# Kernel optimization log

Measured on AMD Instinct MI355X. Metric: run time of the kernel, lower is better.

The kernel has to match this reference:

```python
import jax, jax.numpy as jnp
import numpy as np

NUM_HEADS = 16


def setup_inputs() -> dict:
    key = jax.random.key(0)
    ks = jax.random.split(key, 6)
    B, T, C = 2, 1024, 2048
    H, D = NUM_HEADS, C // NUM_HEADS
    Tc = 1024  # cached tokens
    return {
        "x": jax.random.normal(ks[0], (B, T, C), dtype=jnp.float32),
        "cache_k": jax.random.normal(ks[1], (B, H, Tc, D), dtype=jnp.float32),
        "cache_v": jax.random.normal(ks[2], (B, H, Tc, D), dtype=jnp.float32),
        "W_qkv": jax.random.normal(ks[3], (C, 3 * C), dtype=jnp.float32) * (C ** -0.5),
        "W_proj": jax.random.normal(ks[4], (C, C), dtype=jnp.float32) * (C ** -0.5),
        "b_proj": jnp.zeros((C,), dtype=jnp.float32),
        "seq_start": Tc,
    }


def reference(x, cache_k, cache_v, W_qkv, W_proj, b_proj, seq_start):
    B, T, C = x.shape
    H = NUM_HEADS
    D = C // H
    scale = D ** -0.5

    qkv = (x @ W_qkv).reshape(B, T, 3, H, D)
    # (B, H, T, D)
    q = jnp.transpose(qkv[:, :, 0], (0, 2, 1, 3))
    k = jnp.transpose(qkv[:, :, 1], (0, 2, 1, 3))
    v = jnp.transpose(qkv[:, :, 2], (0, 2, 1, 3))

    # append to KV cache along time axis
    k = jnp.concatenate([cache_k, k], axis=2)
    v = jnp.concatenate([cache_v, v], axis=2)
    k_len = k.shape[2]

    # causal mask on absolute positions: query_pos >= key_pos
    query_pos = seq_start + jnp.arange(T)
    key_pos = jnp.arange(k_len)
    causal = query_pos[:, None] >= key_pos[None, :]  # (T, k_len)

    attn = jnp.einsum("bhqd,bhkd->bhqk", q * scale, k)
    attn = jnp.where(causal[None, None], attn, -jnp.inf)
    attn = jax.nn.softmax(attn, axis=-1)

    out = jnp.einsum("bhqk,bhkd->bhqd", attn, v)
    out = jnp.transpose(out, (0, 2, 1, 3)).reshape(B, T, C)
    out = out @ W_proj + b_proj
    return out, k, v
```

## Files before the change

### kernel.cpp

```cpp
#include <hip/hip_runtime.h>
#include <hip/hip_bf16.h>

typedef __attribute__((ext_vector_type(8))) short bf16x8;
typedef __attribute__((ext_vector_type(4))) float f32x4;
typedef __attribute__((ext_vector_type(16))) float f32x16;

#define DI __device__ __forceinline__

static constexpr int Bb  = 2;
static constexpr int Tt  = 1024;
static constexpr int Cc  = 2048;
static constexpr int Hh  = 16;
static constexpr int Dd  = 128;
static constexpr int TC  = 1024;
static constexpr int CTX = 2048;
static constexpr int LDP = 2112;
static constexpr int VS  = 2080;
static constexpr float QSCALE = 0.08838834764831845f;

DI unsigned short f2bf(float f){
  unsigned u = __builtin_bit_cast(unsigned, f);
  u += 0x7FFFu + ((u >> 16) & 1u);
  return (unsigned short)(u >> 16);
}
DI float bf2f(unsigned short s){
  return __builtin_bit_cast(float, (unsigned)s << 16);
}
DI unsigned pk2(float a, float b){
  return (unsigned)f2bf(a) | ((unsigned)f2bf(b) << 16);
}
DI bf16x8 mk4(unsigned a, unsigned b, unsigned c, unsigned d){
  union{ unsigned u[4]; bf16x8 v; } x;
  x.u[0]=a; x.u[1]=b; x.u[2]=c; x.u[3]=d; return x.v;
}
DI f32x16 mfma32(bf16x8 a, bf16x8 b, f32x16 c){
  return __builtin_amdgcn_mfma_f32_32x32x16_bf16(a, b, c, 0, 0, 0);
}
#define MFMA16(a,b,c) __builtin_amdgcn_mfma_f32_16x16x32_bf16(a,b,c,0,0,0)
DI void gld16(const void* g, void* l){
  __builtin_amdgcn_global_load_lds(
      (const __attribute__((address_space(1))) unsigned int*)g,
      (__attribute__((address_space(3))) unsigned int*)l, 16, 0, 0);
}
DI unsigned ldsoff(const void* p){
  return (unsigned)(size_t)(const __attribute__((address_space(3))) void*)p;
}
template<int OFF>
DI bf16x8 dsr(unsigned addr){
  bf16x8 v;
  if constexpr (OFF == 0)
    asm volatile("ds_read_b128 %0, %1" : "=v"(v) : "v"(addr));
  else
    asm volatile("ds_read_b128 %0, %1 offset:%2" : "=v"(v) : "v"(addr), "i"(OFF));
  return v;
}
#define BARNC   asm volatile("s_barrier")
#define LGKM0   asm volatile("s_waitcnt lgkmcnt(0)")
#define VMCNT4  asm volatile("s_waitcnt vmcnt(4)")
#define VMCNT0  asm volatile("s_waitcnt vmcnt(0)")
#define SBAR    __builtin_amdgcn_sched_barrier(0)

DI void transpose_body(const float* in, unsigned short* out,
                       int R, int C, int ostride, int r0, int c0, int mode,
                       unsigned short (*tile)[33]){
  int tx = threadIdx.x & 31, ty = threadIdx.x >> 5;
#pragma unroll
  for(int i=0;i<4;i++){
    int r = r0 + ty + i*8;
    tile[ty + i*8][tx] = f2bf(in[(size_t)r * C + c0 + tx]);
  }
  __syncthreads();
#pragma unroll
  for(int i=0;i<4;i++){
    int c = c0 + ty + i*8;
    int k = r0 + tx;
    int kp;
    if(mode == 0)
      kp = (k & ~24) | ((((k>>3)&3) ^ ((c>>1)&3)) << 3);
    else
      kp = (k & ~56) | ((((k>>3)&7) ^ (c&7)) << 3);
    out[(size_t)c * ostride + kp] = tile[tx][ty + i*8];
  }
}

__global__ __launch_bounds__(256) void fused_pre_k(
    const float* __restrict__ W_qkv, unsigned short* __restrict__ WqkvT,
    const float4* __restrict__ x4, unsigned short* __restrict__ xbf,
    const float4* __restrict__ ck, const float4* __restrict__ cv,
    float4* __restrict__ ok, float4* __restrict__ ov,
    unsigned short* __restrict__ Kws){
  __shared__ unsigned short tile[32][33];
  int bid = blockIdx.x;
  if(bid < 12288){
    int bx = bid % 192, by = bid / 192;
    transpose_body(W_qkv, WqkvT, 2048, 6144, LDP, by*32, bx*32, 0, tile);
  } else if(bid < 16384){
    int idx = (bid - 12288) * 256 + threadIdx.x;
    int m = idx >> 9;
    int c4 = (idx & 511) * 4;
    float4 v = x4[idx];
    int cp = (c4 & ~24) | ((((c4>>3)&3) ^ ((m>>1)&3)) << 3);
    uint2 p; p.x = pk2(v.x, v.y); p.y = pk2(v.z, v.w);
    *(uint2*)(xbf + (size_t)m * LDP + cp) = p;
  } else {
    int idx = (bid - 16384) * 256 + threadIdx.x;
    const int per = TC * Dd / 4;
    int bh = idx / per, r = idx - bh * per;
    int dst = bh * (CTX * Dd / 4) + r;
    float4 kv = ck[idx];
    ok[dst] = kv;
    ov[dst] = cv[idx];
    int key = r >> 5, dq = (r & 31) * 4;
    int dp = (((dq>>3) ^ (key&7)) << 3) | (dq & 7);
    uint2 p; p.x = pk2(kv.x, kv.y); p.y = pk2(kv.z, kv.w);
    *(uint2*)(Kws + ((size_t)bh * CTX + key) * Dd + dp) = p;
  }
}

__global__ __launch_bounds__(256) void fused_mid_k(
    const float* __restrict__ out_v, unsigned short* __restrict__ Vt_ws,
    const float* __restrict__ W_proj, unsigned short* __restrict__ WprojT){
  __shared__ unsigned short tile[32][33];
  int bid = blockIdx.x;
  if(bid < 8192){
    int z = bid >> 8, rem = bid & 255;
    int bx = rem & 3, by = rem >> 2;
    transpose_body(out_v + (size_t)z*2048*128, Vt_ws + (size_t)z*128*VS,
                   2048, 128, VS, by*32, bx*32, 1, tile);
  } else {
    int b2 = bid - 8192;
    int bx = b2 & 63, by = b2 >> 6;
    transpose_body(W_proj, WprojT, 2048, 2048, LDP, by*32, bx*32, 0, tile);
  }
}

template<int EPI, int NT>
__global__ __launch_bounds__(256, 4) void gemm_t(
    const unsigned short* __restrict__ A, const unsigned short* __restrict__ BT,
    unsigned short* __restrict__ q_ws, float* __restrict__ out_k,
    float* __restrict__ out_v, unsigned short* __restrict__ Kws,
    const float* __restrict__ bias, float* __restrict__ outp){
  constexpr int K = 2048;
  __shared__ unsigned short Al[2][128*32];
  __shared__ unsigned short Bl[2][128*32];
  int tid = threadIdx.x, lane = tid & 63, w = tid >> 6;
  int lr = lane & 15, lg = lane >> 4;
  constexpr int NWG = 16 * NT;
  int bid = blockIdx.x;
  int swz = (bid & 7) * (NWG/8) + (bid >> 3);
  int m0 = (swz & 15) * 128;
  int n0 = (swz >> 4) * 128;
  int wr = (w >> 1) * 64, wc = (w & 1) * 64;
  int fsw = (lg ^ ((lr >> 1) & 3)) << 3;

  unsigned baseAb = ldsoff(Al) + (unsigned)(((wr + lr)*32 + fsw)*2);
  unsigned baseBb = ldsoff(Bl) + (unsigned)(((wc + lr)*32 + fsw)*2);

  f32x4 acc[4][4];
#pragma unroll
  for(int i=0;i<4;i++)
#pragma unroll
    for(int j=0;j<4;j++) acc[i][j] = (f32x4){0.f,0.f,0.f,0.f};

  auto stage = [&](int buf, int k0){
#pragma unroll
    for(int li=0; li<2; li++){
      int rb = w*32 + li*16;
      gld16(A  + (size_t)(m0 + rb + (lane>>2))*LDP + k0 + (lane&3)*8, &Al[buf][rb*32]);
      gld16(BT + (size_t)(n0 + rb + (lane>>2))*LDP + k0 + (lane&3)*8, &Bl[buf][rb*32]);
    }
  };
  stage(0, 0);
  int buf = 0;
#pragma unroll 1
  for(int k0 = 0; k0 < K; k0 += 32){
    SBAR;
    if(k0 + 32 < K){
      stage(buf^1, k0 + 32);
      SBAR;
      VMCNT4;
    } else {
      SBAR;
      VMCNT0;
    }
    BARNC;
    unsigned aA = baseAb + (unsigned)buf*8192u;
    unsigned aB = baseBb + (unsigned)buf*8192u;
    bf16x8 af[4], bfr[4];
    af[0]  = dsr<0>(aA);    af[1]  = dsr<1024>(aA);
    af[2]  = dsr<2048>(aA); af[3]  = dsr<3072>(aA);
    bfr[0] = dsr<0>(aB);    bfr[1] = dsr<1024>(aB);
    bfr[2] = dsr<2048>(aB); bfr[3] = dsr<3072>(aB);
    LGKM0;
    SBAR;
    __builtin_amdgcn_s_setprio(1);
#pragma unroll
    for(int mi=0;mi<4;mi++)
#pragma unroll
      for(int ni=0;ni<4;ni++)
        acc[mi][ni] = MFMA16(af[mi], bfr[ni], acc[mi][ni]);
    __builtin_amdgcn_s_setprio(0);
    SBAR;
    BARNC;
    buf ^= 1;
  }

#pragma unroll
  for(int mi=0;mi<4;mi++){
#pragma unroll
    for(int ni=0;ni<4;ni++){
      int n = n0 + wc + ni*16 + lr;
#pragma unroll
      for(int r=0;r<4;r++){
        int mrow = m0 + wr + mi*16 + lg*4 + r;
        float v = acc[mi][ni][r];
        if constexpr (EPI == 0){
          int seg = n >> 11;
          int h = (n >> 7) & 15, d = n & 127;
          int b = mrow >> 10, t = mrow & 1023;
          if(seg == 0){
            q_ws[((size_t)(b*Hh + h)*Tt + t)*Dd + d] = f2bf(v * QSCALE);
          } else if(seg == 1){
            int key = TC + t;
            size_t base = (size_t)(b*Hh + h)*CTX + key;
            out_k[base*Dd + d] = v;
            int dp = (((d>>3) ^ (key&7)) << 3) | (d & 7);
            Kws[base*Dd + dp] = f2bf(v);
          } else {
            out_v[((size_t)(b*Hh + h)*CTX + TC + t)*Dd + d] = v;
          }
        } else {
          outp[(size_t)mrow * Cc + n] = v + bias[n];
        }
      }
    }
  }
}

__global__ __launch_bounds__(256, 2) void attn_k(
    const unsigned short* __restrict__ q_ws,
    const unsigned short* __restrict__ Kws,
    const unsigned short* __restrict__ Vt,
    float* __restrict__ O0, unsigned short* __restrict__ O1b,
    float* __restrict__ ml){
  __shared__ unsigned short Kl[2][64*128];
  __shared__ unsigned short Vl[2][128*64];
  int tid = threadIdx.x, lane = tid & 63, w = tid >> 6;
  int l31 = lane & 31, hi = lane >> 5, r7 = l31 & 7;
  int qt = blockIdx.x, split = blockIdx.y, bh = blockIdx.z;
  int q0b = qt * 128, qw0 = q0b + w * 32;
  const unsigned short* Kb = Kws + (size_t)bh * CTX * Dd;
  const unsigned short* Vb = Vt  + (size_t)bh * Dd * VS;

  const unsigned short* qp = q_ws + ((size_t)bh * Tt + qw0 + l31) * Dd + hi * 8;
  bf16x8 qf[8];
#pragma unroll
  for(int ks=0;ks<8;ks++) qf[ks] = *(const bf16x8*)(qp + ks*16);

  f32x16 o[4];
#pragma unroll
  for(int dt=0;dt<4;dt++)
#pragma unroll
    for(int r=0;r<16;r++) o[dt][r] = 0.f;
  float m = -3e38f, l = 0.f;

  int nts = ((TC + q0b + 128) >> 6) >> 1;

  auto stageK = [&](int buf, int j0){
#pragma unroll
    for(int li=0; li<4; li++){
      gld16(Kb + (size_t)(j0 + w*16 + li*4 + (lane>>4))*Dd + (lane&15)*8,
            &Kl[buf][(w*16 + li*4)*128]);
    }
  };
  auto stageV = [&](int buf, int j0){
#pragma unroll
    for(int li=0; li<4; li++){
      gld16(Vb + (size_t)(w*32 + li*8 + (lane>>3))*VS + j0 + (lane&7)*8,
            &Vl[buf][(w*32 + li*8)*64]);
    }
  };

  stageK(0, split*64); stageV(0, split*64);
  __syncthreads();
  int buf = 0;
#pragma unroll 1
  for(int t = 0; t < nts; t++){
    int j0 = (2*t + split) * 64;
    if(t + 1 < nts){ stageK(buf^1, j0 + 128); stageV(buf^1, j0 + 128); }

    if(j0 <= TC + qw0 + 31){
      f32x16 s0, s1;
#pragma unroll
      for(int r=0;r<16;r++){ s0[r] = 0.f; s1[r] = 0.f; }
#pragma unroll
      for(int ks=0; ks<8; ks++){
        int ub = ((ks*2 + hi) ^ r7) << 3;
        bf16x8 kf0 = *(const bf16x8*)&Kl[buf][l31*128 + ub];
        bf16x8 kf1 = *(const bf16x8*)&Kl[buf][(32+l31)*128 + ub];
        s0 = mfma32(kf0, qf[ks], s0);
        s1 = mfma32(kf1, qf[ks], s1);
      }
      int qabs = TC + qw0 + l31;
      if(j0 + 63 > TC + qw0){
#pragma unroll
        for(int r=0;r<16;r++){
          int kk = (r&3) + 8*(r>>2) + 4*hi;
          if(j0 + kk > qabs)      s0[r] = -1e30f;
          if(j0 + 32 + kk > qabs) s1[r] = -1e30f;
        }
      }
      float tm = fmaxf(s0[0], s1[0]);
#pragma unroll
      for(int r=1;r<16;r++) tm = fmaxf(tm, fmaxf(s0[r], s1[r]));
      tm = fmaxf(tm, __shfl_xor(tm, 32, 64));
      if(!__all(tm - m <= 8.f)){
        float mn = fmaxf(m, tm);
        float alpha = __expf(m - mn);
        m = mn;
        l *= alpha;
        float ar[16];
#pragma unroll
        for(int r=0;r<16;r++){
          int kk = (r&3) + 8*(r>>2) + 4*hi;
          ar[r] = __shfl(alpha, kk, 64);
        }
#pragma unroll
        for(int dt=0;dt<4;dt++)
#pragma unroll
          for(int r=0;r<16;r++) o[dt][r] *= ar[r];
      }
#pragma unroll
      for(int r=0;r<16;r++){ s0[r] = __expf(s0[r] - m); s1[r] = __expf(s1[r] - m); }
      float ts = 0.f;
#pragma unroll
      for(int r=0;r<16;r++) ts += s0[r] + s1[r];
      ts += __shfl_xor(ts, 32, 64);
      l += ts;
#pragma unroll
      for(int ks16=0; ks16<4; ks16++){
        f32x16 p = (ks16 & 2) ? s1 : s0;
        int fb = (ks16 & 1) * 8;
        unsigned e0 = pk2(p[fb+0], p[fb+1]);
        unsigned e1 = pk2(p[fb+2], p[fb+3]);
        unsigned e2 = pk2(p[fb+4], p[fb+5]);
        unsigned e3 = pk2(p[fb+6], p[fb+7]);
        unsigned x0 = __shfl_xor(e0, 32, 64);
        unsigned x1 = __shfl_xor(e1, 32, 64);
        unsigned x2 = __shfl_xor(e2, 32, 64);
        unsigned x3 = __shfl_xor(e3, 32, 64);
        bf16x8 pa = mk4(hi ? x2 : e0, hi ? x3 : e1, hi ? e2 : x0, hi ? e3 : x1);
        int ub = ((ks16*2 + hi) ^ r7) << 3;
#pragma unroll
        for(int dt=0; dt<4; dt++){
          bf16x8 vf = *(const bf16x8*)&Vl[buf][(dt*32 + l31)*64 + ub];
          o[dt] = mfma32(pa, vf, o[dt]);
        }
      }
    }
    __syncthreads();
    buf ^= 1;
  }

  if(split == 0){
#pragma unroll
    for(int dt=0; dt<4; dt++)
#pragma unroll
      for(int r=0; r<16; r++){
        int q = qw0 + (r&3) + 8*(r>>2) + 4*hi;
        O0[((size_t)bh*Tt + q)*Dd + dt*32 + l31] = o[dt][r];
      }
  } else {
#pragma unroll
    for(int dt=0; dt<4; dt++)
#pragma unroll
      for(int r=0; r<16; r++){
        int q = qw0 + (r&3) + 8*(r>>2) + 4*hi;
        O1b[((size_t)bh*Tt + q)*Dd + dt*32 + l31] = f2bf(o[dt][r]);
      }
  }
  if(lane < 32){
    float* mlp = ml + (((size_t)split*32 + bh)*Tt + qw0 + l31)*2;
    mlp[0] = m; mlp[1] = l;
  }
}

__global__ __launch_bounds__(256) void combine_k(
    const float* __restrict__ O0, const unsigned short* __restrict__ O1b,
    const float* __restrict__ ml, unsigned short* __restrict__ attn_ws){
  int tid = threadIdx.x;
  int d = tid & 127, rl = tid >> 7;
  int row = blockIdx.x * 2 + rl;
  int bh = row >> 10, t = row & 1023;
  const float* p0 = ml + ((size_t)bh * Tt + t) * 2;
  const float* p1 = ml + (((size_t)32 + bh) * Tt + t) * 2;
  float m0 = p0[0], l0 = p0[1], m1 = p1[0], l1 = p1[1];
  float M = fmaxf(m0, m1);
  float e0 = __expf(m0 - M), e1 = __expf(m1 - M);
  float inv = 1.f / (l0*e0 + l1*e1);
  size_t off = (size_t)row * Dd + d;
  float v = (O0[off]*e0 + bf2f(O1b[off])*e1) * inv;
  int b = bh >> 4, h = bh & 15;
  int mrow = b * Tt + t;
  int c = h * Dd + d;
  int cp = (c & ~24) | ((((c>>3)&3) ^ ((mrow>>1)&3)) << 3);
  attn_ws[(size_t)mrow * LDP + cp] = f2bf(v);
}

extern "C" void kernel_launch(void* const* d_in, const int* in_sizes, int n_in,
                              void* d_out, int out_size, void* d_ws, size_t ws_size,
                              hipStream_t stream){
  const float* x       = (const float*)d_in[0];
  const float* cache_k = (const float*)d_in[1];
  const float* cache_v = (const float*)d_in[2];
  const float* W_qkv   = (const float*)d_in[3];
  const float* W_proj  = (const float*)d_in[4];
  const float* b_proj  = (const float*)d_in[5];

  float* out   = (float*)d_out;
  float* out_k = out   + (size_t)Bb*Tt*Cc;
  float* out_v = out_k + (size_t)Bb*Hh*CTX*Dd;

  if(ws_size < (size_t)67108864) return;
  char* ws = (char*)d_ws;
  unsigned short* WqkvT  = (unsigned short*)(ws);
  unsigned short* Vt_ws  = (unsigned short*)(ws);
  unsigned short* attn_ws= (unsigned short*)(ws);
  unsigned short* WprojT = (unsigned short*)(ws + 17039360);
  unsigned short* Kws    = (unsigned short*)(ws + 25952256);
  unsigned short* q_ws   = (unsigned short*)(ws + 42729472);
  unsigned short* x_bf   = (unsigned short*)(ws + 51118080);
  unsigned short* O1b    = (unsigned short*)(ws + 51118080);
  float*          ml     = (float*)(ws + 59768832);
  float*          O0     = out;

  fused_pre_k<<<dim3(20480), 256, 0, stream>>>(
      W_qkv, WqkvT, (const float4*)x, x_bf,
      (const float4*)cache_k, (const float4*)cache_v,
      (float4*)out_k, (float4*)out_v, Kws);
  gemm_t<0,48><<<dim3(768), 256, 0, stream>>>(x_bf, WqkvT, q_ws, out_k, out_v, Kws,
                                              nullptr, nullptr);
  fused_mid_k<<<dim3(12288), 256, 0, stream>>>(out_v, Vt_ws, W_proj, WprojT);
  attn_k<<<dim3(8,2,32), 256, 0, stream>>>(q_ws, Kws, Vt_ws, O0, O1b, ml);
  combine_k<<<dim3(16384), 256, 0, stream>>>(O0, O1b, ml, attn_ws);
  gemm_t<1,16><<<dim3(256), 256, 0, stream>>>(attn_ws, WprojT, nullptr, nullptr, nullptr,
                                              nullptr, b_proj, out);
}
```

Measured before the change: 209.5 us.

## Fold cache copy and transposes into QKV GEMM launch and retile projection GEMM

Moves the KV-cache copy, the W_proj transpose and the cached-V transpose into extra blocks of the QKV GEMM launch, and has the GEMM epilogue write the new V rows directly into a transposed bf16 buffer. This removes the separate mid kernel and its second pass over out_v. The padded leading dimensions (LDP, VS) are dropped in favour of unpadded strides, and the V-transpose buffer now lives in the output region. The projection GEMM uses 64x128 tiles so it launches 512 blocks instead of 256, trading occupancy for smaller tiles. Unpadded strides can cause more LDS or channel conflicts, and the extra blocks compete with the GEMM tiles for CUs.

```diff
diff --git a/kernel.cpp b/kernel.cpp
--- a/kernel.cpp
+++ b/kernel.cpp
@@ -14,8 +14,6 @@
 static constexpr int Dd  = 128;
 static constexpr int TC  = 1024;
 static constexpr int CTX = 2048;
-static constexpr int LDP = 2112;
-static constexpr int VS  = 2080;
 static constexpr float QSCALE = 0.08838834764831845f;
 
 DI unsigned short f2bf(float f){
@@ -57,11 +55,12 @@
 #define BARNC   asm volatile("s_barrier")
 #define LGKM0   asm volatile("s_waitcnt lgkmcnt(0)")
 #define VMCNT4  asm volatile("s_waitcnt vmcnt(4)")
+#define VMCNT3  asm volatile("s_waitcnt vmcnt(3)")
 #define VMCNT0  asm volatile("s_waitcnt vmcnt(0)")
 #define SBAR    __builtin_amdgcn_sched_barrier(0)
 
 DI void transpose_body(const float* in, unsigned short* out,
-                       int R, int C, int ostride, int r0, int c0, int mode,
+                       int C, int ostride, int r0, int c0, int mode,
                        unsigned short (*tile)[33]){
   int tx = threadIdx.x & 31, ty = threadIdx.x >> 5;
 #pragma unroll
@@ -85,68 +84,67 @@
 
 __global__ __launch_bounds__(256) void fused_pre_k(
     const float* __restrict__ W_qkv, unsigned short* __restrict__ WqkvT,
-    const float4* __restrict__ x4, unsigned short* __restrict__ xbf,
-    const float4* __restrict__ ck, const float4* __restrict__ cv,
-    float4* __restrict__ ok, float4* __restrict__ ov,
-    unsigned short* __restrict__ Kws){
+    const float4* __restrict__ x4, unsigned short* __restrict__ xbf){
   __shared__ unsigned short tile[32][33];
   int bid = blockIdx.x;
   if(bid < 12288){
     int bx = bid % 192, by = bid / 192;
-    transpose_body(W_qkv, WqkvT, 2048, 6144, LDP, by*32, bx*32, 0, tile);
-  } else if(bid < 16384){
+    transpose_body(W_qkv, WqkvT, 6144, 2048, by*32, bx*32, 0, tile);
+  } else {
     int idx = (bid - 12288) * 256 + threadIdx.x;
     int m = idx >> 9;
     int c4 = (idx & 511) * 4;
     float4 v = x4[idx];
     int cp = (c4 & ~24) | ((((c4>>3)&3) ^ ((m>>1)&3)) << 3);
     uint2 p; p.x = pk2(v.x, v.y); p.y = pk2(v.z, v.w);
-    *(uint2*)(xbf + (size_t)m * LDP + cp) = p;
-  } else {
-    int idx = (bid - 16384) * 256 + threadIdx.x;
-    const int per = TC * Dd / 4;
-    int bh = idx / per, r = idx - bh * per;
-    int dst = bh * (CTX * Dd / 4) + r;
-    float4 kv = ck[idx];
-    ok[dst] = kv;
-    ov[dst] = cv[idx];
-    int key = r >> 5, dq = (r & 31) * 4;
-    int dp = (((dq>>3) ^ (key&7)) << 3) | (dq & 7);
-    uint2 p; p.x = pk2(kv.x, kv.y); p.y = pk2(kv.z, kv.w);
-    *(uint2*)(Kws + ((size_t)bh * CTX + key) * Dd + dp) = p;
-  }
-}
-
-__global__ __launch_bounds__(256) void fused_mid_k(
-    const float* __restrict__ out_v, unsigned short* __restrict__ Vt_ws,
-    const float* __restrict__ W_proj, unsigned short* __restrict__ WprojT){
-  __shared__ unsigned short tile[32][33];
-  int bid = blockIdx.x;
-  if(bid < 8192){
-    int z = bid >> 8, rem = bid & 255;
-    int bx = rem & 3, by = rem >> 2;
-    transpose_body(out_v + (size_t)z*2048*128, Vt_ws + (size_t)z*128*VS,
-                   2048, 128, VS, by*32, bx*32, 1, tile);
-  } else {
-    int b2 = bid - 8192;
-    int bx = b2 & 63, by = b2 >> 6;
-    transpose_body(W_proj, WprojT, 2048, 2048, LDP, by*32, bx*32, 0, tile);
-  }
-}
-
-template<int EPI, int NT>
-__global__ __launch_bounds__(256, 4) void gemm_t(
+    *(uint2*)(xbf + (size_t)m * Cc + cp) = p;
+  }
+}
+
+__global__ __launch_bounds__(256, 4) void gemmA_k(
     const unsigned short* __restrict__ A, const unsigned short* __restrict__ BT,
     unsigned short* __restrict__ q_ws, float* __restrict__ out_k,
     float* __restrict__ out_v, unsigned short* __restrict__ Kws,
-    const float* __restrict__ bias, float* __restrict__ outp){
-  constexpr int K = 2048;
+    unsigned short* __restrict__ Vt,
+    const float4* __restrict__ ck, const float4* __restrict__ cv,
+    const float* __restrict__ W_proj, unsigned short* __restrict__ WprojT){
   __shared__ unsigned short Al[2][128*32];
   __shared__ unsigned short Bl[2][128*32];
-  int tid = threadIdx.x, lane = tid & 63, w = tid >> 6;
+  int bid = blockIdx.x;
+  int tid = threadIdx.x;
+
+  if(bid >= 768){
+    if(bid < 4864){
+      int idx = (bid - 768) * 256 + tid;
+      const int per = TC * Dd / 4;
+      int bh = idx / per, r = idx - bh * per;
+      int dst = bh * (CTX * Dd / 4) + r;
+      float4 kv = ck[idx];
+      ((float4*)out_k)[dst] = kv;
+      ((float4*)out_v)[dst] = cv[idx];
+      int key = r >> 5, dq = (r & 31) * 4;
+      int dp = (((dq>>3) ^ (key&7)) << 3) | (dq & 7);
+      uint2 p; p.x = pk2(kv.x, kv.y); p.y = pk2(kv.z, kv.w);
+      *(uint2*)(Kws + ((size_t)bh * CTX + key) * Dd + dp) = p;
+    } else if(bid < 8960){
+      int b2 = bid - 4864;
+      int bx = b2 & 63, by = b2 >> 6;
+      transpose_body(W_proj, WprojT, 2048, 2048, by*32, bx*32, 0,
+                     (unsigned short(*)[33])&Al[0][0]);
+    } else {
+      int zz = bid - 8960;
+      int bh = zz >> 7, rem = zz & 127;
+      int bx = rem & 3, by = rem >> 2;
+      transpose_body((const float*)cv + (size_t)bh*131072,
+                     Vt + (size_t)bh*262144, 128, CTX, by*32, bx*32, 1,
+                     (unsigned short(*)[33])&Al[0][0]);
+    }
+    return;
+  }
+
+  int lane = tid & 63, w = tid >> 6;
   int lr = lane & 15, lg = lane >> 4;
-  constexpr int NWG = 16 * NT;
-  int bid = blockIdx.x;
+  constexpr int NWG = 768;
   int swz = (bid & 7) * (NWG/8) + (bid >> 3);
   int m0 = (swz & 15) * 128;
   int n0 = (swz >> 4) * 128;
@@ -166,16 +164,16 @@
 #pragma unroll
     for(int li=0; li<2; li++){
       int rb = w*32 + li*16;
-      gld16(A  + (size_t)(m0 + rb + (lane>>2))*LDP + k0 + (lane&3)*8, &Al[buf][rb*32]);
-      gld16(BT + (size_t)(n0 + rb + (lane>>2))*LDP + k0 + (lane&3)*8, &Bl[buf][rb*32]);
+      gld16(A  + (size_t)(m0 + rb + (lane>>2))*Cc + k0 + (lane&3)*8, &Al[buf][rb*32]);
+      gld16(BT + (size_t)(n0 + rb + (lane>>2))*Cc + k0 + (lane&3)*8, &Bl[buf][rb*32]);
     }
   };
   stage(0, 0);
   int buf = 0;
 #pragma unroll 1
-  for(int k0 = 0; k0 < K; k0 += 32){
+  for(int k0 = 0; k0 < Cc; k0 += 32){
     SBAR;
-    if(k0 + 32 < K){
+    if(k0 + 32 < Cc){
       stage(buf^1, k0 + 32);
       SBAR;
       VMCNT4;
@@ -210,28 +208,107 @@
 #pragma unroll
     for(int ni=0;ni<4;ni++){
       int n = n0 + wc + ni*16 + lr;
+      int seg = n >> 11;
+      int h = (n >> 7) & 15, d = n & 127;
 #pragma unroll
       for(int r=0;r<4;r++){
         int mrow = m0 + wr + mi*16 + lg*4 + r;
         float v = acc[mi][ni][r];
-        if constexpr (EPI == 0){
-          int seg = n >> 11;
-          int h = (n >> 7) & 15, d = n & 127;
-          int b = mrow >> 10, t = mrow & 1023;
-          if(seg == 0){
-            q_ws[((size_t)(b*Hh + h)*Tt + t)*Dd + d] = f2bf(v * QSCALE);
-          } else if(seg == 1){
-            int key = TC + t;
-            size_t base = (size_t)(b*Hh + h)*CTX + key;
-            out_k[base*Dd + d] = v;
-            int dp = (((d>>3) ^ (key&7)) << 3) | (d & 7);
-            Kws[base*Dd + dp] = f2bf(v);
-          } else {
-            out_v[((size_t)(b*Hh + h)*CTX + TC + t)*Dd + d] = v;
-          }
+        int b = mrow >> 10, t = mrow & 1023;
+        if(seg == 0){
+          q_ws[((size_t)(b*Hh + h)*Tt + t)*Dd + d] = f2bf(v * QSCALE);
+        } else if(seg == 1){
+          int key = TC + t;
+          size_t base = (size_t)(b*Hh + h)*CTX + key;
+          out_k[base*Dd + d] = v;
+          int dp = (((d>>3) ^ (key&7)) << 3) | (d & 7);
+          Kws[base*Dd + dp] = f2bf(v);
         } else {
-          outp[(size_t)mrow * Cc + n] = v + bias[n];
+          int key = TC + t;
+          out_v[((size_t)(b*Hh + h)*CTX + key)*Dd + d] = v;
+          int kp = (key & ~56) | ((((key>>3)&7) ^ (d&7)) << 3);
+          Vt[(size_t)(b*Hh + h)*(Dd*CTX) + (size_t)d*CTX + kp] = f2bf(v);
         }
+      }
+    }
+  }
+}
+
+__global__ __launch_bounds__(256, 4) void gemmp_k(
+    const unsigned short* __restrict__ A, const unsigned short* __restrict__ BT,
+    const float* __restrict__ bias, float* __restrict__ outp){
+  __shared__ unsigned short Al[2][64*32];
+  __shared__ unsigned short Bl[2][128*32];
+  int tid = threadIdx.x, lane = tid & 63, w = tid >> 6;
+  int lr = lane & 15, lg = lane >> 4;
+  int bid = blockIdx.x;
+  int swz = (bid & 7) * 64 + (bid >> 3);
+  int m0 = (swz & 31) * 64;
+  int n0 = (swz >> 5) * 128;
+  int wm2 = (w >> 1) * 32, wn2 = (w & 1) * 64;
+  int fsw = (lg ^ ((lr >> 1) & 3)) << 3;
+
+  unsigned baseAb = ldsoff(Al) + (unsigned)(((wm2 + lr)*32 + fsw)*2);
+  unsigned baseBb = ldsoff(Bl) + (unsigned)(((wn2 + lr)*32 + fsw)*2);
+
+  f32x4 acc[2][4];
+#pragma unroll
+  for(int i=0;i<2;i++)
+#pragma unroll
+    for(int j=0;j<4;j++) acc[i][j] = (f32x4){0.f,0.f,0.f,0.f};
+
+  auto stage = [&](int buf, int k0){
+    gld16(A + (size_t)(m0 + w*16 + (lane>>2))*Cc + k0 + (lane&3)*8,
+          &Al[buf][w*16*32]);
+#pragma unroll
+    for(int li=0; li<2; li++){
+      int rb = w*32 + li*16;
+      gld16(BT + (size_t)(n0 + rb + (lane>>2))*Cc + k0 + (lane&3)*8, &Bl[buf][rb*32]);
+    }
+  };
+  stage(0, 0);
+  int buf = 0;
+#pragma unroll 1
+  for(int k0 = 0; k0 < Cc; k0 += 32){
+    SBAR;
+    if(k0 + 32 < Cc){
+      stage(buf^1, k0 + 32);
+      SBAR;
+      VMCNT3;
+    } else {
+      SBAR;
+      VMCNT0;
+    }
+    BARNC;
+    unsigned aA = baseAb + (unsigned)buf*4096u;
+    unsigned aB = baseBb + (unsigned)buf*8192u;
+    bf16x8 af[2], bfr[4];
+    af[0]  = dsr<0>(aA);    af[1]  = dsr<1024>(aA);
+    bfr[0] = dsr<0>(aB);    bfr[1] = dsr<1024>(aB);
+    bfr[2] = dsr<2048>(aB); bfr[3] = dsr<3072>(aB);
+    LGKM0;
+    SBAR;
+    __builtin_amdgcn_s_setprio(1);
+#pragma unroll
+    for(int mi=0;mi<2;mi++)
+#pragma unroll
+      for(int ni=0;ni<4;ni++)
+        acc[mi][ni] = MFMA16(af[mi], bfr[ni], acc[mi][ni]);
+    __builtin_amdgcn_s_setprio(0);
+    SBAR;
+    BARNC;
+    buf ^= 1;
+  }
+
+#pragma unroll
+  for(int mi=0;mi<2;mi++){
+#pragma unroll
+    for(int ni=0;ni<4;ni++){
+      int n = n0 + wn2 + ni*16 + lr;
+#pragma unroll
+      for(int r=0;r<4;r++){
+        int mrow = m0 + wm2 + mi*16 + lg*4 + r;
+        outp[(size_t)mrow * Cc + n] = acc[mi][ni][r] + bias[n];
       }
     }
   }
@@ -250,7 +327,7 @@
   int qt = blockIdx.x, split = blockIdx.y, bh = blockIdx.z;
   int q0b = qt * 128, qw0 = q0b + w * 32;
   const unsigned short* Kb = Kws + (size_t)bh * CTX * Dd;
-  const unsigned short* Vb = Vt  + (size_t)bh * Dd * VS;
+  const unsigned short* Vb = Vt  + (size_t)bh * Dd * CTX;
 
   const unsigned short* qp = q_ws + ((size_t)bh * Tt + qw0 + l31) * Dd + hi * 8;
   bf16x8 qf[8];
@@ -276,7 +353,7 @@
   auto stageV = [&](int buf, int j0){
 #pragma unroll
     for(int li=0; li<4; li++){
-      gld16(Vb + (size_t)(w*32 + li*8 + (lane>>3))*VS + j0 + (lane&7)*8,
+      gld16(Vb + (size_t)(w*32 + li*8 + (lane>>3))*CTX + j0 + (lane&7)*8,
             &Vl[buf][(w*32 + li*8)*64]);
     }
   };
@@ -404,7 +481,7 @@
   int mrow = b * Tt + t;
   int c = h * Dd + d;
   int cp = (c & ~24) | ((((c>>3)&3) ^ ((mrow>>1)&3)) << 3);
-  attn_ws[(size_t)mrow * LDP + cp] = f2bf(v);
+  attn_ws[(size_t)mrow * Cc + cp] = f2bf(v);
 }
 
 extern "C" void kernel_launch(void* const* d_in, const int* in_sizes, int n_in,
@@ -420,29 +497,25 @@
   float* out   = (float*)d_out;
   float* out_k = out   + (size_t)Bb*Tt*Cc;
   float* out_v = out_k + (size_t)Bb*Hh*CTX*Dd;
+  unsigned short* Vt = (unsigned short*)out;
 
   if(ws_size < (size_t)67108864) return;
   char* ws = (char*)d_ws;
   unsigned short* WqkvT  = (unsigned short*)(ws);
-  unsigned short* Vt_ws  = (unsigned short*)(ws);
-  unsigned short* attn_ws= (unsigned short*)(ws);
-  unsigned short* WprojT = (unsigned short*)(ws + 17039360);
-  unsigned short* Kws    = (unsigned short*)(ws + 25952256);
-  unsigned short* q_ws   = (unsigned short*)(ws + 42729472);
-  unsigned short* x_bf   = (unsigned short*)(ws + 51118080);
-  unsigned short* O1b    = (unsigned short*)(ws + 51118080);
-  float*          ml     = (float*)(ws + 59768832);
-  float*          O0     = out;
-
-  fused_pre_k<<<dim3(20480), 256, 0, stream>>>(
-      W_qkv, WqkvT, (const float4*)x, x_bf,
-      (const float4*)cache_k, (const float4*)cache_v,
-      (float4*)out_k, (float4*)out_v, Kws);
-  gemm_t<0,48><<<dim3(768), 256, 0, stream>>>(x_bf, WqkvT, q_ws, out_k, out_v, Kws,
-                                              nullptr, nullptr);
-  fused_mid_k<<<dim3(12288), 256, 0, stream>>>(out_v, Vt_ws, W_proj, WprojT);
-  attn_k<<<dim3(8,2,32), 256, 0, stream>>>(q_ws, Kws, Vt_ws, O0, O1b, ml);
+  float*          O0     = (float*)(ws);
+  float*          ml     = (float*)(ws + 16777216);
+  unsigned short* WprojT = (unsigned short*)(ws + 25165824);
+  unsigned short* Kws    = (unsigned short*)(ws + 33554432);
+  unsigned short* attn_ws= (unsigned short*)(ws + 33554432);
+  unsigned short* q_ws   = (unsigned short*)(ws + 50331648);
+  unsigned short* x_bf   = (unsigned short*)(ws + 58720256);
+  unsigned short* O1b    = (unsigned short*)(ws + 58720256);
+
+  fused_pre_k<<<dim3(16384), 256, 0, stream>>>(W_qkv, WqkvT, (const float4*)x, x_bf);
+  gemmA_k<<<dim3(13056), 256, 0, stream>>>(x_bf, WqkvT, q_ws, out_k, out_v, Kws, Vt,
+                                           (const float4*)cache_k, (const float4*)cache_v,
+                                           W_proj, WprojT);
+  attn_k<<<dim3(8,2,32), 256, 0, stream>>>(q_ws, Kws, Vt, O0, O1b, ml);
   combine_k<<<dim3(16384), 256, 0, stream>>>(O0, O1b, ml, attn_ws);
-  gemm_t<1,16><<<dim3(256), 256, 0, stream>>>(attn_ws, WprojT, nullptr, nullptr, nullptr,
-                                              nullptr, b_proj, out);
-}
+  gemmp_k<<<dim3(512), 256, 0, stream>>>(attn_ws, WprojT, b_proj, out);
+}
```

Measured after the change: 202.0 us. -3.6%, faster.
